# Optimization experiments

Measured on AMD Instinct MI355X. Metric: run time of the kernel, lower is better.

Reference implementation:

```python
import math
import jax, jax.numpy as jnp
import numpy as np


def _tokenformer_theta(scores):
    # L2-normalize along last dim, scale by sqrt(n), then exact GELU (torch F.gelu default)
    n = scores.shape[-1]
    l2 = jnp.maximum(jnp.linalg.norm(scores, ord=2, axis=-1, keepdims=True), 1e-8)
    scaled = scores * (math.sqrt(n) / l2)
    return jax.nn.gelu(scaled, approximate=False)


def setup_inputs() -> dict:
    key = jax.random.key(0)
    k1, k2, k3 = jax.random.split(key, 3)
    B, T, C = 4, 2048, 1024
    heads, num_tokens = 8, 1024
    key_hd, val_hd = C // heads, 1024 // heads
    x = jax.random.normal(k1, (B, T, C), dtype=jnp.float32)
    # kaiming_uniform_(a=sqrt(5)) on [heads, num_tokens, head_dim]: bound = sqrt(6/((1+5)*fan_in)) = 1/sqrt(fan_in)
    bk = 1.0 / math.sqrt(num_tokens)
    key_tokens = jax.random.uniform(k2, (heads, num_tokens, key_hd), minval=-bk, maxval=bk, dtype=jnp.float32)
    val_tokens = jax.random.uniform(k3, (heads, num_tokens, val_hd), minval=-bk, maxval=bk, dtype=jnp.float32)
    return {"x": x, "key_tokens": key_tokens, "val_tokens": val_tokens}


def reference(x, key_tokens, val_tokens):
    B, T, C = x.shape
    H, N, Dk = key_tokens.shape
    # q: [B, H, T, Dk]
    q = x.reshape(B, T, H, Dk).transpose(0, 2, 1, 3)
    # scores: [B, H, T, N]
    scores = jnp.einsum('bhtd,hnd->bhtn', q, key_tokens)
    scores = _tokenformer_theta(scores)
    # ThresHot: hard hot-mask keeping entries above the per-row mean (straight-through quantizer)
    mask = scores > jnp.mean(scores, axis=-1, keepdims=True)
    scores = jnp.where(mask, scores, 0.0)
    # out: [B, H, T, Dv] -> [B, T, H*Dv]
    out = jnp.einsum('bhtn,hnv->bhtv', scores, val_tokens)
    return out.transpose(0, 2, 1, 3).reshape(B, T, -1)
```

## Files before the change

kernel.cpp:

```cpp
#include <hip/hip_runtime.h>
#include <cstdint>
#include <cmath>


typedef __bf16 bf16x8 __attribute__((ext_vector_type(8)));
typedef float  f32x16 __attribute__((ext_vector_type(16)));
typedef float  f32x4  __attribute__((ext_vector_type(4)));
typedef unsigned short u16x8 __attribute__((ext_vector_type(8)));

#if defined(__has_builtin)
#if __has_builtin(__builtin_amdgcn_cvt_pk_f32_fp8) && __has_builtin(__builtin_amdgcn_cvt_pk_fp8_f32)
#define HW_FP8 1
#endif
#endif
#ifndef HW_FP8
#define HW_FP8 0
#endif

__device__ __forceinline__ unsigned short bfbits(__bf16 b) {
  return __builtin_bit_cast(unsigned short, b);
}

__device__ __forceinline__ void gload_lds16(const void* g, void* l) {
  __builtin_amdgcn_global_load_lds(
      (const __attribute__((address_space(1))) void*)g,
      (__attribute__((address_space(3))) void*)l, 16, 0, 0);
}

__device__ __forceinline__ unsigned int enc_fp8_1(float f) {
  unsigned int u = __float_as_uint(f);
  unsigned int s = u >> 31;
  u &= 0x7FFFFFFFu;
  unsigned int r = (u + 0x7FFFFu + ((u >> 20) & 1u)) >> 20;
  unsigned int mag = (r >= 968u) ? (r - 960u) : 0u;
  if (mag > 127u) mag = 127u;
  return (s << 7) | mag;
}

template <bool WORD>
__device__ __forceinline__ unsigned int pack_fp8_pair(float a, float b,
                                                      unsigned int old) {
#if HW_FP8
  return (unsigned int)__builtin_amdgcn_cvt_pk_fp8_f32(a, b, (int)old, WORD);
#else
  const unsigned int pk = enc_fp8_1(a) | (enc_fp8_1(b) << 8);
  return WORD ? ((old & 0x0000FFFFu) | (pk << 16))
              : ((old & 0xFFFF0000u) | pk);
#endif
}

__device__ __forceinline__ unsigned short dec_fp8_1(unsigned int b) {
  const unsigned int t = b & 0x7Fu;
  unsigned int v = (t << 4) + 14080u;
  v |= (b & 0x80u) << 8;
  return (t >= 16u) ? (unsigned short)v : (unsigned short)0;
}

__device__ __forceinline__ bf16x8 dec_qlo(uint2 lo) {
#if HW_FP8
  const float S = 1.0f / 1024.0f;
  auto p0 = __builtin_amdgcn_cvt_pk_f32_fp8((int)lo.x, false);
  auto p1 = __builtin_amdgcn_cvt_pk_f32_fp8((int)lo.x, true);
  auto p2 = __builtin_amdgcn_cvt_pk_f32_fp8((int)lo.y, false);
  auto p3 = __builtin_amdgcn_cvt_pk_f32_fp8((int)lo.y, true);
  unsigned int w0, w1, w2, w3;
  asm("v_cvt_pk_bf16_f32 %0, %1, %2" : "=v"(w0) : "v"(p0[0] * S), "v"(p0[1] * S));
  asm("v_cvt_pk_bf16_f32 %0, %1, %2" : "=v"(w1) : "v"(p1[0] * S), "v"(p1[1] * S));
  asm("v_cvt_pk_bf16_f32 %0, %1, %2" : "=v"(w2) : "v"(p2[0] * S), "v"(p2[1] * S));
  asm("v_cvt_pk_bf16_f32 %0, %1, %2" : "=v"(w3) : "v"(p3[0] * S), "v"(p3[1] * S));
  uint4 uu = make_uint4(w0, w1, w2, w3);
  return __builtin_bit_cast(bf16x8, uu);
#else
  unsigned short r0 = dec_fp8_1(lo.x & 0xFFu);
  unsigned short r1 = dec_fp8_1((lo.x >> 8) & 0xFFu);
  unsigned short r2 = dec_fp8_1((lo.x >> 16) & 0xFFu);
  unsigned short r3 = dec_fp8_1(lo.x >> 24);
  unsigned short r4 = dec_fp8_1(lo.y & 0xFFu);
  unsigned short r5 = dec_fp8_1((lo.y >> 8) & 0xFFu);
  unsigned short r6 = dec_fp8_1((lo.y >> 16) & 0xFFu);
  unsigned short r7 = dec_fp8_1(lo.y >> 24);
  uint4 uu = make_uint4((unsigned)r0 | ((unsigned)r1 << 16),
                        (unsigned)r2 | ((unsigned)r3 << 16),
                        (unsigned)r4 | ((unsigned)r5 << 16),
                        (unsigned)r6 | ((unsigned)r7 << 16));
  return __builtin_bit_cast(bf16x8, uu);
#endif
}

__device__ __forceinline__ float gelu_s(float raw, float c707, float chalf) {
  const float s = raw * c707;
  const float a = fabsf(s);
  float u = fmaf(a, 4.30638e-5f, 2.765672e-4f);
  u = fmaf(u, a, 1.520143e-4f);
  u = fmaf(u, a, 9.2705272e-3f);
  u = fmaf(u, a, 4.22820123e-2f);
  u = fmaf(u, a, 7.05230784e-2f);
  u = fmaf(u, a, 1.0f);
  const float r  = __builtin_amdgcn_rcpf(u);
  const float r2 = r * r;
  const float r4 = r2 * r2;
  const float r8 = r4 * r4;
  const float er = copysignf(1.0f - r8 * r8, s);
  const float hf = raw * chalf;
  return fmaf(hf, er, hf);
}

__global__ void prep_kv(const float* __restrict__ key,
                        const float* __restrict__ val,
                        unsigned short* __restrict__ kh,
                        unsigned short* __restrict__ kl,
                        unsigned short* __restrict__ vp) {
  const int gid = blockIdx.x * 256 + threadIdx.x;
  if (gid < 65536) {
    const int h = gid >> 13;
    const int s = (gid >> 10) & 7;
    const int n = gid & 1023;
    const float* src = key + ((size_t)(h << 10) + n) * 128 + s * 16;
    float fv[16];
#pragma unroll
    for (int j = 0; j < 4; ++j) {
      const float4 f = *(const float4*)(src + j * 4);
      fv[j * 4 + 0] = f.x; fv[j * 4 + 1] = f.y;
      fv[j * 4 + 2] = f.z; fv[j * 4 + 3] = f.w;
    }
    u16x8 hv0, hv1, lv0, lv1;
#pragma unroll
    for (int e = 0; e < 8; ++e) {
      const __bf16 hb0 = (__bf16)fv[e];
      hv0[e] = bfbits(hb0);
      lv0[e] = bfbits((__bf16)(fv[e] - (float)hb0));
      const __bf16 hb1 = (__bf16)fv[8 + e];
      hv1[e] = bfbits(hb1);
      lv1[e] = bfbits((__bf16)(fv[8 + e] - (float)hb1));
    }
    const size_t o = ((size_t)(h * 8 + s) * 1024 + n) * 16;
    *(u16x8*)(kh + o) = hv0;  *(u16x8*)(kh + o + 8) = hv1;
    *(u16x8*)(kl + o) = lv0;  *(u16x8*)(kl + o + 8) = lv1;
  } else {
    const int tid = gid - 65536;
    const int h   = tid >> 14;
    const int s2  = (tid >> 7) & 127;
    const int v   = tid & 127;
    const float* src = val + ((size_t)(h << 10) + s2 * 8) * 128 + v;
    u16x8 ov;
#pragma unroll
    for (int e = 0; e < 8; ++e) ov[e] = bfbits((__bf16)src[(size_t)e * 128]);
    *(u16x8*)(vp + ((size_t)(h * 128 + s2) * 128 + v) * 8) = ov;
  }
}

#define QHI_OFF 131072
#define QLO_OFF 147456
#define RED_OFF 155648
#define SMEMSZ  159744

__global__ __launch_bounds__(1024, 4) void fused_mhk(
    const float* __restrict__ x,
    const unsigned short* __restrict__ k_hi,
    const unsigned short* __restrict__ k_lo,
    const unsigned short* __restrict__ v_pk,
    float* __restrict__ out)
{
  extern __shared__ char smem[];
  const int tid  = threadIdx.x;
  const int wave = tid >> 6;
  const int lane = tid & 63;
  const int l31  = lane & 31;
  const int hi   = lane >> 5;

  const int bid = blockIdx.x;
  const int h   = bid & 7;
  const int g8  = bid >> 3;
  const int b   = g8 & 3;
  const int tt  = g8 >> 2;
  const int t0  = tt * 64;

  const unsigned short* kh2 = k_hi + (size_t)h * 131072;
  const unsigned short* kl2 = k_lo + (size_t)h * 131072;
  float* red = (float*)(smem + RED_OFF);

  {
    const float* xq = x + ((size_t)(b * 2048 + t0)) * 1024 + h * 128;
    const int r = tid >> 4, kc = tid & 15;
    const float* sp = xq + (size_t)r * 1024 + kc * 8;
    const float4 f0 = *(const float4*)sp;
    const float4 f1 = *(const float4*)(sp + 4);
    const float fv[8] = {f0.x, f0.y, f0.z, f0.w, f1.x, f1.y, f1.z, f1.w};
    bf16x8 hv; float lv[8];
#pragma unroll
    for (int e = 0; e < 8; ++e) {
      const __bf16 hb = (__bf16)fv[e];
      hv[e] = hb;
      lv[e] = (fv[e] - (float)hb) * 1024.0f;
    }
    const int g = kc * 64 + (r ^ ((kc >> 1) & 7));
    *(bf16x8*)(smem + QHI_OFF + g * 16) = hv;
    unsigned int w0 = pack_fp8_pair<false>(lv[0], lv[1], 0u);
    w0 = pack_fp8_pair<true>(lv[2], lv[3], w0);
    unsigned int w1 = pack_fp8_pair<false>(lv[4], lv[5], 0u);
    w1 = pack_fp8_pair<true>(lv[6], lv[7], w1);
    *(uint2*)(smem + QLO_OFF + g * 8) = make_uint2(w0, w1);
  }
  {
    const unsigned short* sh = kh2 + wave * 1024 + lane * 8;
    const unsigned short* sl = kl2 + wave * 1024 + lane * 8;
    gload_lds16(sh,       smem + wave * 2048);
    gload_lds16(sh + 512, smem + wave * 2048 + 1024);
    gload_lds16(sl,       smem + 32768 + wave * 2048);
    gload_lds16(sl + 512, smem + 32768 + wave * 2048 + 1024);
  }
  __syncthreads();

  f32x16 acc[2][2];
#pragma unroll
  for (int t = 0; t < 2; ++t)
#pragma unroll
    for (int qt = 0; qt < 2; ++qt)
#pragma unroll
      for (int e = 0; e < 16; ++e) acc[t][qt][e] = 0.f;

#pragma unroll
  for (int s = 0; s < 8; ++s) {
    if (s < 7) {
      char* nxt = smem + ((s + 1) & 1) * 65536;
      const unsigned short* sh = kh2 + (s + 1) * 16384 + wave * 1024 + lane * 8;
      const unsigned short* sl = kl2 + (s + 1) * 16384 + wave * 1024 + lane * 8;
      gload_lds16(sh,       nxt + wave * 2048);
      gload_lds16(sh + 512, nxt + wave * 2048 + 1024);
      gload_lds16(sl,       nxt + 32768 + wave * 2048);
      gload_lds16(sl + 512, nxt + 32768 + wave * 2048 + 1024);
    }
    const char* cur = smem + (s & 1) * 65536;
    const int gx0 = (2 * s + hi) * 64 + (l31 ^ s);
    const int gx1 = (2 * s + hi) * 64 + ((32 + l31) ^ s);
    const bf16x8 bqh0 = *(const bf16x8*)(smem + QHI_OFF + gx0 * 16);
    const bf16x8 bqh1 = *(const bf16x8*)(smem + QHI_OFF + gx1 * 16);
    const bf16x8 bql0 = dec_qlo(*(const uint2*)(smem + QLO_OFF + gx0 * 8));
    const bf16x8 bql1 = dec_qlo(*(const uint2*)(smem + QLO_OFF + gx1 * 8));
    const int na = wave * 64 + l31;
    const bf16x8 ah0 = *(const bf16x8*)(cur + na * 32 + hi * 16);
    const bf16x8 ah1 = *(const bf16x8*)(cur + (na + 32) * 32 + hi * 16);
    const bf16x8 al0 = *(const bf16x8*)(cur + 32768 + na * 32 + hi * 16);
    const bf16x8 al1 = *(const bf16x8*)(cur + 32768 + (na + 32) * 32 + hi * 16);

    acc[0][0] = __builtin_amdgcn_mfma_f32_32x32x16_bf16(ah0, bqh0, acc[0][0], 0, 0, 0);
    acc[0][1] = __builtin_amdgcn_mfma_f32_32x32x16_bf16(ah0, bqh1, acc[0][1], 0, 0, 0);
    acc[0][0] = __builtin_amdgcn_mfma_f32_32x32x16_bf16(ah0, bql0, acc[0][0], 0, 0, 0);
    acc[0][1] = __builtin_amdgcn_mfma_f32_32x32x16_bf16(ah0, bql1, acc[0][1], 0, 0, 0);
    acc[0][0] = __builtin_amdgcn_mfma_f32_32x32x16_bf16(al0, bqh0, acc[0][0], 0, 0, 0);
    acc[0][1] = __builtin_amdgcn_mfma_f32_32x32x16_bf16(al0, bqh1, acc[0][1], 0, 0, 0);
    acc[1][0] = __builtin_amdgcn_mfma_f32_32x32x16_bf16(ah1, bqh0, acc[1][0], 0, 0, 0);
    acc[1][1] = __builtin_amdgcn_mfma_f32_32x32x16_bf16(ah1, bqh1, acc[1][1], 0, 0, 0);
    acc[1][0] = __builtin_amdgcn_mfma_f32_32x32x16_bf16(ah1, bql0, acc[1][0], 0, 0, 0);
    acc[1][1] = __builtin_amdgcn_mfma_f32_32x32x16_bf16(ah1, bql1, acc[1][1], 0, 0, 0);
    acc[1][0] = __builtin_amdgcn_mfma_f32_32x32x16_bf16(al1, bqh0, acc[1][0], 0, 0, 0);
    acc[1][1] = __builtin_amdgcn_mfma_f32_32x32x16_bf16(al1, bqh1, acc[1][1], 0, 0, 0);

    __syncthreads();
  }

  float ss0 = 0.f, ss1 = 0.f;
#pragma unroll
  for (int t = 0; t < 2; ++t)
#pragma unroll
    for (int e = 0; e < 16; ++e) {
      ss0 += acc[t][0][e] * acc[t][0][e];
      ss1 += acc[t][1][e] * acc[t][1][e];
    }
  ss0 += __shfl_xor(ss0, 32);
  ss1 += __shfl_xor(ss1, 32);
  red[wave * 64 + lane] = hi ? ss1 : ss0;
  __syncthreads();
  float sum0 = 0.f, sum1 = 0.f;
#pragma unroll
  for (int w = 0; w < 16; ++w) {
    sum0 += red[w * 64 + l31];
    sum1 += red[w * 64 + 32 + l31];
  }
  const float scale0 = 32.0f / fmaxf(sqrtf(sum0), 1e-8f);
  const float scale1 = 32.0f / fmaxf(sqrtf(sum1), 1e-8f);
  const float c707_0 = scale0 * 0.70710678118654752f;
  const float c707_1 = scale1 * 0.70710678118654752f;
  const float chalf0 = scale0 * 0.5f;
  const float chalf1 = scale1 * 0.5f;

  float gs0 = 0.f, gs1 = 0.f;
#pragma unroll
  for (int t = 0; t < 2; ++t)
#pragma unroll
    for (int e = 0; e < 16; ++e) {
      const float g0 = gelu_s(acc[t][0][e], c707_0, chalf0);
      acc[t][0][e] = g0; gs0 += g0;
      const float g1 = gelu_s(acc[t][1][e], c707_1, chalf1);
      acc[t][1][e] = g1; gs1 += g1;
    }
  gs0 += __shfl_xor(gs0, 32);
  gs1 += __shfl_xor(gs1, 32);
  __syncthreads();
  red[wave * 64 + lane] = hi ? gs1 : gs0;
  __syncthreads();
  float mean0 = 0.f, mean1 = 0.f;
#pragma unroll
  for (int w = 0; w < 16; ++w) {
    mean0 += red[w * 64 + l31];
    mean1 += red[w * 64 + 32 + l31];
  }
  mean0 *= (1.0f / 1024.0f);
  mean1 *= (1.0f / 1024.0f);

#pragma unroll
  for (int t = 0; t < 2; ++t) {
#pragma unroll
    for (int qt = 0; qt < 2; ++qt) {
      const float mn = qt ? mean1 : mean0;
      const int q = qt * 32 + l31;
#pragma unroll
      for (int gi = 0; gi < 4; ++gi) {
        float g0 = acc[t][qt][4 * gi + 0]; g0 = (g0 > mn) ? g0 : 0.f;
        float g1 = acc[t][qt][4 * gi + 1]; g1 = (g1 > mn) ? g1 : 0.f;
        float g2 = acc[t][qt][4 * gi + 2]; g2 = (g2 > mn) ? g2 : 0.f;
        float g3 = acc[t][qt][4 * gi + 3]; g3 = (g3 > mn) ? g3 : 0.f;
        uint2 pk;
        pk.x = (unsigned)bfbits((__bf16)g0) | ((unsigned)bfbits((__bf16)g1) << 16);
        pk.y = (unsigned)bfbits((__bf16)g2) | ((unsigned)bfbits((__bf16)g3) << 16);
        const int ng = wave * 8 + t * 4 + gi;
        const int swz = (t * 4 + gi) & 7;
        *(uint2*)(smem + (ng * 64 + (q ^ swz)) * 16 + hi * 8) = pk;
      }
    }
  }
  __syncthreads();

  if (wave >= 8) return;
  const int qt2 = wave >> 2;
  const int vt  = wave & 3;
  const int q   = qt2 * 32 + l31;

  f32x16 o;
#pragma unroll
  for (int e = 0; e < 16; ++e) o[e] = 0.f;

  const unsigned short* vb = v_pk + (size_t)h * 131072 + (size_t)hi * 1024 +
                             (size_t)(vt * 32 + l31) * 8;
#pragma unroll 8
  for (int ks = 0; ks < 64; ++ks) {
    const int ng = 2 * ks + hi;
    const bf16x8 aa = *(const bf16x8*)(smem + (ng * 64 + (q ^ (ng & 7))) * 16);
    const bf16x8 bb = *(const bf16x8*)(vb + (size_t)ks * 2048);
    o = __builtin_amdgcn_mfma_f32_32x32x16_bf16(aa, bb, o, 0, 0, 0);
  }

  float* op = out + ((size_t)(b * 2048 + t0 + qt2 * 32)) * 1024 +
              h * 128 + vt * 32 + l31;
#pragma unroll
  for (int r = 0; r < 16; ++r) {
    const int qr = (r & 3) + 8 * (r >> 2) + 4 * hi;
    op[(size_t)qr * 1024] = o[r];
  }
}


extern "C" void kernel_launch(void* const* d_in, const int* in_sizes, int n_in,
                              void* d_out, int out_size, void* d_ws, size_t ws_size,
                              hipStream_t stream) {
  const float* x   = (const float*)d_in[0];
  const float* key = (const float*)d_in[1];
  const float* val = (const float*)d_in[2];
  float* out = (float*)d_out;

  if (ws_size < (size_t)6 * 1024 * 1024) return;

  unsigned short* k_hi = (unsigned short*)d_ws;
  unsigned short* k_lo = k_hi + 1048576;
  unsigned short* v_pk = k_lo + 1048576;

  prep_kv<<<dim3(768), dim3(256), 0, stream>>>(key, val, k_hi, k_lo, v_pk);
  fused_mhk<<<dim3(1024), dim3(1024), SMEMSZ, stream>>>(x, k_hi, k_lo, v_pk, out);
}
```

Baseline: 121.0 us.

## Drop per-stage block barrier, prefetch V operand, pack GELU math

In the score loop each wave now reads only the LDS slice it loaded itself. The per-stage __syncthreads is therefore replaced by an explicit s_waitcnt vmcnt on that wave's own global_load_lds ops, plus a sched_barrier. MFMA sections are raised in priority with s_setprio. The GELU epilogue is rewritten on 2-wide float vectors to encourage packed FP32 ops, and the V-operand global load in the second GEMM is software-prefetched one iteration ahead. These target barrier stalls, exposed global-load latency and ALU cost in the epilogue, at the cost of relying on exact vmcnt counting for correctness.

Result: faster. 113.1 us (-6.5%).

```diff
diff --git a/kernel.cpp b/kernel.cpp
--- a/kernel.cpp
+++ b/kernel.cpp
@@ -5,7 +5,7 @@
 
 typedef __bf16 bf16x8 __attribute__((ext_vector_type(8)));
 typedef float  f32x16 __attribute__((ext_vector_type(16)));
-typedef float  f32x4  __attribute__((ext_vector_type(4)));
+typedef float  f32x2  __attribute__((ext_vector_type(2)));
 typedef unsigned short u16x8 __attribute__((ext_vector_type(8)));
 
 #if defined(__has_builtin)
@@ -87,22 +87,24 @@
 #endif
 }
 
-__device__ __forceinline__ float gelu_s(float raw, float c707, float chalf) {
-  const float s = raw * c707;
-  const float a = fabsf(s);
-  float u = fmaf(a, 4.30638e-5f, 2.765672e-4f);
-  u = fmaf(u, a, 1.520143e-4f);
-  u = fmaf(u, a, 9.2705272e-3f);
-  u = fmaf(u, a, 4.22820123e-2f);
-  u = fmaf(u, a, 7.05230784e-2f);
-  u = fmaf(u, a, 1.0f);
-  const float r  = __builtin_amdgcn_rcpf(u);
-  const float r2 = r * r;
-  const float r4 = r2 * r2;
-  const float r8 = r4 * r4;
-  const float er = copysignf(1.0f - r8 * r8, s);
-  const float hf = raw * chalf;
-  return fmaf(hf, er, hf);
+__device__ __forceinline__ f32x2 gelu2(f32x2 raw, float c707, float chalf) {
+  const f32x2 s = raw * c707;
+  const f32x2 a = __builtin_elementwise_abs(s);
+  f32x2 u = a * 4.30638e-5f + 2.765672e-4f;
+  u = __builtin_elementwise_fma(u, a, (f32x2)1.520143e-4f);
+  u = __builtin_elementwise_fma(u, a, (f32x2)9.2705272e-3f);
+  u = __builtin_elementwise_fma(u, a, (f32x2)4.22820123e-2f);
+  u = __builtin_elementwise_fma(u, a, (f32x2)7.05230784e-2f);
+  u = __builtin_elementwise_fma(u, a, (f32x2)1.0f);
+  f32x2 r;
+  r.x = __builtin_amdgcn_rcpf(u.x);
+  r.y = __builtin_amdgcn_rcpf(u.y);
+  const f32x2 r2 = r * r;
+  const f32x2 r4 = r2 * r2;
+  const f32x2 r8 = r4 * r4;
+  const f32x2 er = __builtin_elementwise_copysign((f32x2)1.0f - r8 * r8, s);
+  const f32x2 hf = raw * chalf;
+  return __builtin_elementwise_fma(hf, er, hf);
 }
 
 __global__ void prep_kv(const float* __restrict__ key,
@@ -229,7 +231,12 @@
       gload_lds16(sh + 512, nxt + wave * 2048 + 1024);
       gload_lds16(sl,       nxt + 32768 + wave * 2048);
       gload_lds16(sl + 512, nxt + 32768 + wave * 2048 + 1024);
-    }
+      asm volatile("s_waitcnt vmcnt(4)" ::: "memory");
+    } else {
+      asm volatile("s_waitcnt vmcnt(0)" ::: "memory");
+    }
+    __builtin_amdgcn_sched_barrier(0);
+
     const char* cur = smem + (s & 1) * 65536;
     const int gx0 = (2 * s + hi) * 64 + (l31 ^ s);
     const int gx1 = (2 * s + hi) * 64 + ((32 + l31) ^ s);
@@ -243,6 +250,7 @@
     const bf16x8 al0 = *(const bf16x8*)(cur + 32768 + na * 32 + hi * 16);
     const bf16x8 al1 = *(const bf16x8*)(cur + 32768 + (na + 32) * 32 + hi * 16);
 
+    __builtin_amdgcn_s_setprio(1);
     acc[0][0] = __builtin_amdgcn_mfma_f32_32x32x16_bf16(ah0, bqh0, acc[0][0], 0, 0, 0);
     acc[0][1] = __builtin_amdgcn_mfma_f32_32x32x16_bf16(ah0, bqh1, acc[0][1], 0, 0, 0);
     acc[0][0] = __builtin_amdgcn_mfma_f32_32x32x16_bf16(ah0, bql0, acc[0][0], 0, 0, 0);
@@ -255,8 +263,7 @@
     acc[1][1] = __builtin_amdgcn_mfma_f32_32x32x16_bf16(ah1, bql1, acc[1][1], 0, 0, 0);
     acc[1][0] = __builtin_amdgcn_mfma_f32_32x32x16_bf16(al1, bqh0, acc[1][0], 0, 0, 0);
     acc[1][1] = __builtin_amdgcn_mfma_f32_32x32x16_bf16(al1, bqh1, acc[1][1], 0, 0, 0);
-
-    __syncthreads();
+    __builtin_amdgcn_s_setprio(0);
   }
 
   float ss0 = 0.f, ss1 = 0.f;
@@ -288,11 +295,15 @@
 #pragma unroll
   for (int t = 0; t < 2; ++t)
 #pragma unroll
-    for (int e = 0; e < 16; ++e) {
-      const float g0 = gelu_s(acc[t][0][e], c707_0, chalf0);
-      acc[t][0][e] = g0; gs0 += g0;
-      const float g1 = gelu_s(acc[t][1][e], c707_1, chalf1);
-      acc[t][1][e] = g1; gs1 += g1;
+    for (int e = 0; e < 16; e += 2) {
+      f32x2 in0; in0.x = acc[t][0][e]; in0.y = acc[t][0][e + 1];
+      const f32x2 g0 = gelu2(in0, c707_0, chalf0);
+      acc[t][0][e] = g0.x; acc[t][0][e + 1] = g0.y;
+      gs0 += g0.x + g0.y;
+      f32x2 in1; in1.x = acc[t][1][e]; in1.y = acc[t][1][e + 1];
+      const f32x2 g1 = gelu2(in1, c707_1, chalf1);
+      acc[t][1][e] = g1.x; acc[t][1][e + 1] = g1.y;
+      gs1 += g1.x + g1.y;
     }
   gs0 += __shfl_xor(gs0, 32);
   gs1 += __shfl_xor(gs1, 32);
@@ -342,12 +353,15 @@
 
   const unsigned short* vb = v_pk + (size_t)h * 131072 + (size_t)hi * 1024 +
                              (size_t)(vt * 32 + l31) * 8;
+  bf16x8 vcur = *(const bf16x8*)(vb);
 #pragma unroll 8
   for (int ks = 0; ks < 64; ++ks) {
     const int ng = 2 * ks + hi;
     const bf16x8 aa = *(const bf16x8*)(smem + (ng * 64 + (q ^ (ng & 7))) * 16);
-    const bf16x8 bb = *(const bf16x8*)(vb + (size_t)ks * 2048);
-    o = __builtin_amdgcn_mfma_f32_32x32x16_bf16(aa, bb, o, 0, 0, 0);
+    bf16x8 vn;
+    if (ks < 63) vn = *(const bf16x8*)(vb + (size_t)(ks + 1) * 2048);
+    o = __builtin_amdgcn_mfma_f32_32x32x16_bf16(aa, vcur, o, 0, 0, 0);
+    if (ks < 63) vcur = vn;
   }
 
   float* op = out + ((size_t)(b * 2048 + t0 + qt2 * 32)) * 1024 +
```
